# Optimization experiments

Measured on AMD Instinct MI355X. Metric: run time of the kernel, lower is better.

## Reference

```python
import jax, jax.numpy as jnp
import numpy as np

N = 200000      # nodes
E = 200000      # edges per direction
IN = 256        # in_dim
HID = 256       # hidden_dim
HEADS = 4
C = HID // HEADS  # 64 per-head channels
OUT = 128
EPS = 1e-5      # LayerNorm eps (torch default)


def _ln(x, g, b):
    m = jnp.mean(x, axis=-1, keepdims=True)
    v = jnp.mean(jnp.square(x - m), axis=-1, keepdims=True)
    return (x - m) / jnp.sqrt(v + EPS) * g + b


def _gat(x, W, att_src, att_dst, bias, edge_index):
    """PyG GATConv (default args: add_self_loops=True, negative_slope=0.2, concat heads)."""
    n = x.shape[0]
    loops = jnp.arange(n, dtype=edge_index.dtype)
    ei = jnp.concatenate([edge_index, jnp.stack([loops, loops])], axis=1)
    src, dst = ei[0], ei[1]
    h = (x @ W).reshape(n, HEADS, C)                      # [N,H,C]
    a_src = jnp.sum(h * att_src, axis=-1)                 # [N,H]
    a_dst = jnp.sum(h * att_dst, axis=-1)                 # [N,H]
    e = jax.nn.leaky_relu(a_src[src] + a_dst[dst], 0.2)   # [E+N,H]
    m = jax.ops.segment_max(e, dst, num_segments=n)       # per-dst softmax max
    ex = jnp.exp(e - m[dst])
    denom = jax.ops.segment_sum(ex, dst, num_segments=n)
    alpha = ex / denom[dst]                               # [E+N,H]
    out = jax.ops.segment_sum(h[src] * alpha[..., None], dst, num_segments=n)
    return out.reshape(n, HEADS * C) + bias


def setup_inputs() -> dict:
    key = jax.random.key(0)
    ks = jax.random.split(key, 20)
    w = lambda k, s, sc=0.05: jax.random.normal(k, s, jnp.float32) * sc
    return {
        "x": jax.random.normal(ks[0], (N, IN), jnp.float32),
        "edge_index_bu": jax.random.randint(ks[1], (2, E), 0, N, jnp.int32),
        "edge_index_td": jax.random.randint(ks[2], (2, E), 0, N, jnp.int32),
        "Wp": w(ks[3], (IN, HID)), "bp": jnp.zeros((HID,), jnp.float32),
        "W_bu": w(ks[4], (HID, HID)), "asrc_bu": w(ks[5], (HEADS, C)),
        "adst_bu": w(ks[6], (HEADS, C)), "bias_bu": jnp.zeros((HID,), jnp.float32),
        "W_td": w(ks[7], (HID, HID)), "asrc_td": w(ks[8], (HEADS, C)),
        "adst_td": w(ks[9], (HEADS, C)), "bias_td": jnp.zeros((HID,), jnp.float32),
        "Wf": w(ks[10], (2 * HID, OUT)), "bf": jnp.zeros((OUT,), jnp.float32),
        "g_bu": jnp.ones((HID,), jnp.float32), "b_bu": jnp.zeros((HID,), jnp.float32),
        "g_td": jnp.ones((HID,), jnp.float32), "b_td": jnp.zeros((HID,), jnp.float32),
        "g_out": jnp.ones((OUT,), jnp.float32), "b_out": jnp.zeros((OUT,), jnp.float32),
    }


def reference(x, edge_index_bu, edge_index_td, Wp, bp,
              W_bu, asrc_bu, adst_bu, bias_bu,
              W_td, asrc_td, adst_td, bias_td,
              Wf, bf, g_bu, b_bu, g_td, b_td, g_out, b_out):
    h = jax.nn.relu(x @ Wp + bp)  # dropout is identity in eval
    x_bu = jax.nn.relu(_ln(_gat(h, W_bu, asrc_bu, adst_bu, bias_bu, edge_index_bu), g_bu, b_bu))
    x_td = jax.nn.relu(_ln(_gat(h, W_td, asrc_td, adst_td, bias_td, edge_index_td), g_td, b_td))
    out = jnp.concatenate([x_bu, x_td], axis=-1) @ Wf + bf
    out = _ln(out, g_out, b_out)
    nrm = jnp.sqrt(jnp.sum(jnp.square(out), axis=-1, keepdims=True))
    return out / jnp.maximum(nrm, 1e-12)
```

## Files before the change

### kernel.cpp

```cpp
#include <hip/hip_runtime.h>
#include <hip/hip_bf16.h>
#include <stdint.h>


typedef __attribute__((ext_vector_type(8))) short bf16x8;
typedef __attribute__((ext_vector_type(4))) short bf16x4;
typedef __attribute__((ext_vector_type(4))) float f32x4;

#define HID 256

__device__ __forceinline__ float red16(float v) {
    #pragma unroll
    for (int o = 1; o < 16; o <<= 1) v += __shfl_xor(v, o, 64);
    return v;
}
__device__ __forceinline__ float bf2f(short s) {
    return __uint_as_float(((unsigned)(unsigned short)s) << 16);
}

__device__ __forceinline__ void gload_lds16(const void* g, void* l) {
    __builtin_amdgcn_global_load_lds(
        reinterpret_cast<const __attribute__((address_space(1))) uint32_t*>(
            reinterpret_cast<uintptr_t>(g)),
        reinterpret_cast<__attribute__((address_space(3))) uint32_t*>(
            reinterpret_cast<uintptr_t>(l)),
        16, 0, 0);
}

__global__ void transpose_w(const float* __restrict__ W,
                            __hip_bfloat16* __restrict__ Wt, int KI, int KO) {
    int idx = blockIdx.x * 256 + threadIdx.x;
    if (idx >= KI * KO) return;
    int k = idx / KO, j = idx % KO;
    Wt[(long)j * KI + k] = __float2bfloat16(W[idx]);
}

template<int BN, int MODE, int CVT>
__global__ __launch_bounds__(512) void gemm_tiled(
    const float* __restrict__ Af, const __hip_bfloat16* __restrict__ Ab, int lda,
    const __hip_bfloat16* __restrict__ Bt, int KI,
    const float* __restrict__ bias, int doRelu,
    __hip_bfloat16* __restrict__ outB, int ldcB, int colOff,
    float* __restrict__ outF,
    const float* __restrict__ gw, const float* __restrict__ bw, int N) {

    constexpr int WN = BN / 64;
    constexpr int WM = 8 / WN;
    constexpr int MR = (128 / WM) / 16;

    __shared__ __align__(16) __hip_bfloat16 sA[2][128 * 32];
    __shared__ __align__(16) __hip_bfloat16 sB[2][BN * 32];
    __shared__ float sRed[MODE == 2 ? 128 * 4 : 4];
    __shared__ float sN2[MODE == 2 ? 128 * 2 : 2];

    int tid = threadIdx.x;
    int wv = tid >> 6, ln = tid & 63;
    int m = ln & 15, q = ln >> 4;
    long row0 = (long)blockIdx.x * 128;
    int wr = (wv / WN) * (128 / WM);
    int wc = (wv % WN) * 64;

    f32x4 acc[MR][4];
    #pragma unroll
    for (int mi = 0; mi < MR; ++mi)
        #pragma unroll
        for (int t = 0; t < 4; ++t) acc[mi][t] = (f32x4){0.f, 0.f, 0.f, 0.f};

    int oA = tid * 16;
    long rowA = row0 + (oA >> 6);
    if (rowA >= N) rowA = N - 1;
    int kel = (oA & 63) >> 1;
    long aBase = rowA * (long)lda + kel;

    auto stage = [&](int buf, int k0) {
        if constexpr (CVT) {
            const float* src = Af + aBase + k0;
            f32x4 fa0 = *(const f32x4*)src;
            f32x4 fa1 = *(const f32x4*)(src + 4);
            __hip_bfloat16 t8[8];
            t8[0] = __float2bfloat16(fa0[0]); t8[1] = __float2bfloat16(fa0[1]);
            t8[2] = __float2bfloat16(fa0[2]); t8[3] = __float2bfloat16(fa0[3]);
            t8[4] = __float2bfloat16(fa1[0]); t8[5] = __float2bfloat16(fa1[1]);
            t8[6] = __float2bfloat16(fa1[2]); t8[7] = __float2bfloat16(fa1[3]);
            *(bf16x8*)((char*)sA[buf] + oA) = *(const bf16x8*)t8;
        } else {
            gload_lds16(Ab + aBase + k0, (char*)sA[buf] + oA);
        }
        #pragma unroll
        for (int j = 0; j < BN / 128; ++j) {
            int o = j * 8192 + tid * 16;
            const __hip_bfloat16* src = Bt + (long)(o >> 6) * KI + k0 + ((o & 63) >> 1);
            gload_lds16(src, (char*)sB[buf] + o);
        }
    };

    auto compute = [&](int buf) {
        bf16x8 af[MR], bfr[4];
        #pragma unroll
        for (int mi = 0; mi < MR; ++mi)
            af[mi] = *(const bf16x8*)((const char*)sA[buf] + ((wr + mi * 16 + m) << 6) + q * 16);
        #pragma unroll
        for (int t = 0; t < 4; ++t)
            bfr[t] = *(const bf16x8*)((const char*)sB[buf] + ((wc + t * 16 + m) << 6) + q * 16);
        #pragma unroll
        for (int mi = 0; mi < MR; ++mi)
            #pragma unroll
            for (int t = 0; t < 4; ++t)
                acc[mi][t] = __builtin_amdgcn_mfma_f32_16x16x32_bf16(af[mi], bfr[t],
                                                                     acc[mi][t], 0, 0, 0);
    };

    stage(0, 0);
    __syncthreads();
    int cur = 0;
    for (int k0 = 0; k0 < KI; k0 += 32) {
        if (k0 + 32 < KI) stage(cur ^ 1, k0 + 32);
        compute(cur);
        __syncthreads();
        cur ^= 1;
    }

    if constexpr (MODE != 2) {
        #pragma unroll
        for (int mi = 0; mi < MR; ++mi) {
            #pragma unroll
            for (int t = 0; t < 4; ++t) {
                int col = wc + t * 16 + m;
                float bv = bias ? bias[col] : 0.f;
                #pragma unroll
                for (int r = 0; r < 4; ++r) {
                    long row = row0 + wr + mi * 16 + q * 4 + r;
                    if (row < N) {
                        float v = acc[mi][t][r] + bv;
                        if (doRelu) v = fmaxf(v, 0.f);
                        outB[row * ldcB + colOff + col] = __float2bfloat16(v);
                    }
                }
            }
        }
    }

    if constexpr (MODE == 2) {
        float vv[MR][4][4];
        float gcol[4], bcol[4];
        #pragma unroll
        for (int t = 0; t < 4; ++t) {
            int col = wc + t * 16 + m;
            float bb = bias[col];
            gcol[t] = gw[col]; bcol[t] = bw[col];
            #pragma unroll
            for (int mi = 0; mi < MR; ++mi)
                #pragma unroll
                for (int r = 0; r < 4; ++r) vv[mi][t][r] = acc[mi][t][r] + bb;
        }
        int wcid = wc >> 6;
        __syncthreads();
        #pragma unroll
        for (int mi = 0; mi < MR; ++mi) {
            #pragma unroll
            for (int r = 0; r < 4; ++r) {
                float s1 = vv[mi][0][r] + vv[mi][1][r] + vv[mi][2][r] + vv[mi][3][r];
                float s2 = vv[mi][0][r] * vv[mi][0][r] + vv[mi][1][r] * vv[mi][1][r]
                         + vv[mi][2][r] * vv[mi][2][r] + vv[mi][3][r] * vv[mi][3][r];
                s1 = red16(s1); s2 = red16(s2);
                if (m == 0) {
                    int lrow = wr + mi * 16 + q * 4 + r;
                    sRed[lrow * 4 + wcid * 2 + 0] = s1;
                    sRed[lrow * 4 + wcid * 2 + 1] = s2;
                }
            }
        }
        __syncthreads();
        #pragma unroll
        for (int mi = 0; mi < MR; ++mi) {
            #pragma unroll
            for (int r = 0; r < 4; ++r) {
                int lrow = wr + mi * 16 + q * 4 + r;
                float S1 = sRed[lrow * 4 + 0] + sRed[lrow * 4 + 2];
                float S2 = sRed[lrow * 4 + 1] + sRed[lrow * 4 + 3];
                float mean = S1 * (1.f / 128.f);
                float var = S2 * (1.f / 128.f) - mean * mean;
                float inv = rsqrtf(fmaxf(var, 0.f) + 1e-5f);
                float n2 = 0.f;
                #pragma unroll
                for (int t = 0; t < 4; ++t) {
                    float y = (vv[mi][t][r] - mean) * inv * gcol[t] + bcol[t];
                    vv[mi][t][r] = y;
                    n2 += y * y;
                }
                n2 = red16(n2);
                if (m == 0) sN2[lrow * 2 + wcid] = n2;
            }
        }
        __syncthreads();
        #pragma unroll
        for (int mi = 0; mi < MR; ++mi) {
            #pragma unroll
            for (int r = 0; r < 4; ++r) {
                int lrow = wr + mi * 16 + q * 4 + r;
                long row = row0 + lrow;
                float nrm = sqrtf(sN2[lrow * 2] + sN2[lrow * 2 + 1]);
                float sc = 1.f / fmaxf(nrm, 1e-12f);
                if (row < N) {
                    #pragma unroll
                    for (int t = 0; t < 4; ++t)
                        outF[row * 128 + wc + t * 16 + m] = vv[mi][t][r] * sc;
                }
            }
        }
    }
}

__global__ __launch_bounds__(1024) void gemm_dir2(
    const __hip_bfloat16* __restrict__ Ab,
    const __hip_bfloat16* __restrict__ Bt,
    const float* __restrict__ asrc0, const float* __restrict__ adst0,
    const float* __restrict__ asrc1, const float* __restrict__ adst1,
    float* __restrict__ aS0, float* __restrict__ aD0,
    float* __restrict__ aS1, float* __restrict__ aD1,
    __hip_bfloat16* __restrict__ outB, int N) {
    constexpr int KI = 256;
    __shared__ __align__(16) __hip_bfloat16 sA[128 * 32];
    __shared__ __align__(16) __hip_bfloat16 sB[512 * 32];

    int tid = threadIdx.x;
    int wv = tid >> 6, ln = tid & 63;
    int m = ln & 15, q = ln >> 4;
    long row0 = (long)blockIdx.x * 128;
    int wr = (wv >> 3) * 64;
    int wc = (wv & 7) * 64;

    f32x4 acc[4][4];
    #pragma unroll
    for (int mi = 0; mi < 4; ++mi)
        #pragma unroll
        for (int t = 0; t < 4; ++t) acc[mi][t] = (f32x4){0.f, 0.f, 0.f, 0.f};

    int oA = (tid & 511) * 16;
    long rowA = row0 + (oA >> 6);
    if (rowA >= N) rowA = N - 1;
    int kel = (oA & 63) >> 1;
    long aBase = rowA * (long)KI + kel;
    int oB0 = tid * 16;
    int kelB = (oB0 & 63) >> 1;

    for (int k0 = 0; k0 < KI; k0 += 32) {
        __syncthreads();
        if (tid < 512) gload_lds16(Ab + aBase + k0, (char*)sA + oA);
        #pragma unroll
        for (int j = 0; j < 2; ++j) {
            int o = j * 16384 + oB0;
            const __hip_bfloat16* src = Bt + (long)(o >> 6) * KI + k0 + ((o & 63) >> 1);
            gload_lds16(src, (char*)sB + o);
        }
        __syncthreads();

        bf16x8 af[4], bfr[4];
        #pragma unroll
        for (int mi = 0; mi < 4; ++mi)
            af[mi] = *(const bf16x8*)((const char*)sA + ((wr + mi * 16 + m) << 6) + q * 16);
        #pragma unroll
        for (int t = 0; t < 4; ++t)
            bfr[t] = *(const bf16x8*)((const char*)sB + ((wc + t * 16 + m) << 6) + q * 16);
        #pragma unroll
        for (int mi = 0; mi < 4; ++mi)
            #pragma unroll
            for (int t = 0; t < 4; ++t)
                acc[mi][t] = __builtin_amdgcn_mfma_f32_16x16x32_bf16(af[mi], bfr[t],
                                                                     acc[mi][t], 0, 0, 0);
    }

    #pragma unroll
    for (int mi = 0; mi < 4; ++mi) {
        #pragma unroll
        for (int t = 0; t < 4; ++t) {
            int col = wc + t * 16 + m;
            #pragma unroll
            for (int r = 0; r < 4; ++r) {
                long row = row0 + wr + mi * 16 + q * 4 + r;
                if (row < N) outB[row * 512 + col] = __float2bfloat16(acc[mi][t][r]);
            }
        }
    }

    int dir = wc >> 8;
    int cc = wc & 255;
    int h = cc >> 6;
    const float* as_ = dir ? asrc1 : asrc0;
    const float* ad_ = dir ? adst1 : adst0;
    float* aS = dir ? aS1 : aS0;
    float* aD = dir ? aD1 : aD0;
    f32x4 sw, dw;
    #pragma unroll
    for (int t = 0; t < 4; ++t) {
        sw[t] = as_[cc + t * 16 + m];
        dw[t] = ad_[cc + t * 16 + m];
    }
    #pragma unroll
    for (int mi = 0; mi < 4; ++mi) {
        #pragma unroll
        for (int r = 0; r < 4; ++r) {
            float ps = acc[mi][0][r] * sw[0] + acc[mi][1][r] * sw[1]
                     + acc[mi][2][r] * sw[2] + acc[mi][3][r] * sw[3];
            float pd = acc[mi][0][r] * dw[0] + acc[mi][1][r] * dw[1]
                     + acc[mi][2][r] * dw[2] + acc[mi][3][r] * dw[3];
            ps = red16(ps); pd = red16(pd);
            long row = row0 + wr + mi * 16 + q * 4 + r;
            if (m == 0 && row < N) {
                aS[row * 4 + h] = ps;
                aD[row * 4 + h] = pd;
            }
        }
    }
}

__global__ __launch_bounds__(256) void hist_dst(const int* __restrict__ ei, int E,
                                                int* __restrict__ cnt) {
    int e = blockIdx.x * 256 + threadIdx.x;
    if (e < E) atomicAdd(&cnt[ei[E + e]], 1);
}

__global__ __launch_bounds__(256) void scan1(const int* __restrict__ cnt,
                                             int* __restrict__ offpart,
                                             int* __restrict__ bsum, int n) {
    int t = threadIdx.x, i = blockIdx.x * 256 + t;
    int lane = t & 63, w = t >> 6;
    int v = (i < n) ? cnt[i] : 0;
    int inc = v;
    #pragma unroll
    for (int o = 1; o < 64; o <<= 1) {
        int u = __shfl_up(inc, o, 64);
        if (lane >= o) inc += u;
    }
    __shared__ int wsum[4];
    if (lane == 63) wsum[w] = inc;
    __syncthreads();
    int wadd = 0;
    #pragma unroll
    for (int k = 0; k < 4; ++k) if (k < w) wadd += wsum[k];
    if (i < n) offpart[i] = inc - v + wadd;
    if (t == 255) bsum[blockIdx.x] = inc + wadd;
}

__global__ __launch_bounds__(256) void scan2(const int* __restrict__ bsum,
                                             int* __restrict__ btot, int nb) {
    int t = threadIdx.x, lane = t & 63, w = t >> 6;
    int loc[4]; int s = 0;
    #pragma unroll
    for (int k = 0; k < 4; ++k) {
        int idx = t * 4 + k;
        int v = (idx < nb) ? bsum[idx] : 0;
        loc[k] = s; s += v;
    }
    int inc = s;
    #pragma unroll
    for (int o = 1; o < 64; o <<= 1) {
        int u = __shfl_up(inc, o, 64);
        if (lane >= o) inc += u;
    }
    __shared__ int wsum[4];
    if (lane == 63) wsum[w] = inc;
    __syncthreads();
    int wadd = 0;
    #pragma unroll
    for (int k = 0; k < 4; ++k) if (k < w) wadd += wsum[k];
    int excl = inc - s + wadd;
    #pragma unroll
    for (int k = 0; k < 4; ++k) {
        int idx = t * 4 + k;
        if (idx < nb) btot[idx] = excl + loc[k];
    }
}

__global__ __launch_bounds__(256) void finalize_off(const int* __restrict__ offpart,
                                                    const int* __restrict__ btot,
                                                    int* __restrict__ off, int n, int E) {
    int i = blockIdx.x * 256 + threadIdx.x;
    if (i < n) off[i] = offpart[i] + btot[i >> 8];
    if (i == 0) off[n] = E;
}

__global__ __launch_bounds__(256) void scatter_src(const int* __restrict__ ei, int E,
                                                   const int* __restrict__ off,
                                                   int* __restrict__ cur,
                                                   int* __restrict__ esrc) {
    int e = blockIdx.x * 256 + threadIdx.x;
    if (e >= E) return;
    int d = ei[E + e];
    int pos = off[d] + atomicAdd(&cur[d], 1);
    esrc[pos] = ei[e];
}

__global__ __launch_bounds__(256) void att_alpha(
    const int* __restrict__ off, const int* __restrict__ esrc,
    const float* __restrict__ a_s, const float* __restrict__ a_d,
    float* __restrict__ alpha_self, float* __restrict__ alpha_e, int N) {
    int d = blockIdx.x * 256 + threadIdx.x;
    if (d >= N) return;
    int beg = off[d], end = off[d + 1];
    f32x4 adv = *(const f32x4*)(a_d + 4 * (long)d);
    f32x4 asd = *(const f32x4*)(a_s + 4 * (long)d);
    float es[4], m[4];
    #pragma unroll
    for (int h = 0; h < 4; ++h) {
        float e = asd[h] + adv[h]; e = e > 0.f ? e : 0.2f * e;
        es[h] = e; m[h] = e;
    }
    for (int j = beg; j < end; ++j) {
        int s = esrc[j];
        f32x4 asv = *(const f32x4*)(a_s + 4 * (long)s);
        #pragma unroll
        for (int h = 0; h < 4; ++h) {
            float e = asv[h] + adv[h]; e = e > 0.f ? e : 0.2f * e;
            m[h] = fmaxf(m[h], e);
        }
    }
    float sum[4];
    #pragma unroll
    for (int h = 0; h < 4; ++h) sum[h] = __expf(es[h] - m[h]);
    for (int j = beg; j < end; ++j) {
        int s = esrc[j];
        f32x4 asv = *(const f32x4*)(a_s + 4 * (long)s);
        #pragma unroll
        for (int h = 0; h < 4; ++h) {
            float e = asv[h] + adv[h]; e = e > 0.f ? e : 0.2f * e;
            sum[h] += __expf(e - m[h]);
        }
    }
    float rs[4];
    #pragma unroll
    for (int h = 0; h < 4; ++h) rs[h] = 1.f / sum[h];
    f32x4 sa;
    #pragma unroll
    for (int h = 0; h < 4; ++h) sa[h] = __expf(es[h] - m[h]) * rs[h];
    *(f32x4*)(alpha_self + 4 * (long)d) = sa;
    for (int j = beg; j < end; ++j) {
        int s = esrc[j];
        f32x4 asv = *(const f32x4*)(a_s + 4 * (long)s);
        f32x4 av;
        #pragma unroll
        for (int h = 0; h < 4; ++h) {
            float e = asv[h] + adv[h]; e = e > 0.f ? e : 0.2f * e;
            av[h] = __expf(e - m[h]) * rs[h];
        }
        *(f32x4*)(alpha_e + 4 * (long)j) = av;
    }
}

__global__ __launch_bounds__(256) void gat_gather(
    const int* __restrict__ off, const int* __restrict__ esrc,
    const float* __restrict__ alpha_self, const float* __restrict__ alpha_e,
    const __hip_bfloat16* __restrict__ hw, int dirOff,
    const float* __restrict__ bias, const float* __restrict__ g,
    const float* __restrict__ b,
    __hip_bfloat16* __restrict__ out, int N) {
    int tid = threadIdx.x;
    int lane = tid & 63;
    int grp = lane >> 4, li = lane & 15;
    long d = (long)blockIdx.x * 16 + (tid >> 6) * 4 + grp;
    if (d >= N) return;
    int beg = off[d], end = off[d + 1];
    int head = li >> 2;
    int c0 = li * 16;
    float acc[16];
    {
        float a = alpha_self[4 * d + head];
        const __hip_bfloat16* r = hw + d * 512 + dirOff + c0;
        bf16x8 h0 = *(const bf16x8*)r;
        bf16x8 h1 = *(const bf16x8*)(r + 8);
        #pragma unroll
        for (int k = 0; k < 8; ++k) {
            acc[k] = a * bf2f(h0[k]);
            acc[8 + k] = a * bf2f(h1[k]);
        }
    }
    for (int j = beg; j < end; ++j) {
        int s = esrc[j];
        float a = alpha_e[4 * (long)j + head];
        const __hip_bfloat16* r = hw + (long)s * 512 + dirOff + c0;
        bf16x8 h0 = *(const bf16x8*)r;
        bf16x8 h1 = *(const bf16x8*)(r + 8);
        #pragma unroll
        for (int k = 0; k < 8; ++k) {
            acc[k] += a * bf2f(h0[k]);
            acc[8 + k] += a * bf2f(h1[k]);
        }
    }
    float s1 = 0.f, s2 = 0.f;
    #pragma unroll
    for (int k = 0; k < 16; k += 4) {
        f32x4 bi = *(const f32x4*)(bias + c0 + k);
        #pragma unroll
        for (int u = 0; u < 4; ++u) {
            float v = acc[k + u] + bi[u];
            acc[k + u] = v;
            s1 += v; s2 += v * v;
        }
    }
    #pragma unroll
    for (int o = 1; o < 16; o <<= 1) {
        s1 += __shfl_xor(s1, o, 64);
        s2 += __shfl_xor(s2, o, 64);
    }
    float mean = s1 * (1.f / 256.f);
    float var = s2 * (1.f / 256.f) - mean * mean;
    float inv = rsqrtf(fmaxf(var, 0.f) + 1e-5f);
    __hip_bfloat16 o16[16];
    #pragma unroll
    for (int k = 0; k < 16; k += 4) {
        f32x4 gv = *(const f32x4*)(g + c0 + k);
        f32x4 bv = *(const f32x4*)(b + c0 + k);
        #pragma unroll
        for (int u = 0; u < 4; ++u) {
            float y = (acc[k + u] - mean) * inv * gv[u] + bv[u];
            o16[k + u] = __float2bfloat16(fmaxf(y, 0.f));
        }
    }
    __hip_bfloat16* orow = out + d * 512 + dirOff + c0;
    *(bf16x8*)orow = *(const bf16x8*)o16;
    *(bf16x8*)(orow + 8) = *(const bf16x8*)(o16 + 8);
}

extern "C" void kernel_launch(void* const* d_in, const int* in_sizes, int n_in,
                              void* d_out, int out_size, void* d_ws, size_t ws_size,
                              hipStream_t stream) {
    const float* x      = (const float*)d_in[0];
    const int*   ei_bu  = (const int*)d_in[1];
    const int*   ei_td  = (const int*)d_in[2];
    const float* Wp     = (const float*)d_in[3];
    const float* bp     = (const float*)d_in[4];
    const float* W_bu   = (const float*)d_in[5];
    const float* asrc_bu= (const float*)d_in[6];
    const float* adst_bu= (const float*)d_in[7];
    const float* bias_bu= (const float*)d_in[8];
    const float* W_td   = (const float*)d_in[9];
    const float* asrc_td= (const float*)d_in[10];
    const float* adst_td= (const float*)d_in[11];
    const float* bias_td= (const float*)d_in[12];
    const float* Wf     = (const float*)d_in[13];
    const float* bfv    = (const float*)d_in[14];
    const float* g_bu   = (const float*)d_in[15];
    const float* b_bu   = (const float*)d_in[16];
    const float* g_td   = (const float*)d_in[17];
    const float* b_td   = (const float*)d_in[18];
    const float* g_out  = (const float*)d_in[19];
    const float* b_out  = (const float*)d_in[20];

    const int N = in_sizes[0] / HID;
    const int E = in_sizes[1] / 2;

    char* ws = (char*)d_ws;
    size_t off0 = 0;
    auto take = [&](size_t bytes) -> char* {
        char* p = ws + off0;
        off0 += (bytes + 255) & ~(size_t)255;
        return p;
    };
    __hip_bfloat16* h_buf = (__hip_bfloat16*)take((size_t)N * 256 * 2);
    __hip_bfloat16* hwcat = (__hip_bfloat16*)take((size_t)N * 512 * 2);
    __hip_bfloat16* xcat  = (__hip_bfloat16*)take((size_t)N * 512 * 2);
    float* aS0   = (float*)take((size_t)N * 16);
    float* aD0   = (float*)take((size_t)N * 16);
    float* aS1   = (float*)take((size_t)N * 16);
    float* aD1   = (float*)take((size_t)N * 16);
    float* alsf  = (float*)take((size_t)N * 16);
    float* ale   = (float*)take((size_t)E * 16);
    int* cnt     = (int*)take((size_t)N * 4);
    int* cur     = (int*)take((size_t)N * 4);
    int* offpart = (int*)take((size_t)N * 4);
    int* offarr  = (int*)take((size_t)(N + 1) * 4);
    int* esrc    = (int*)take((size_t)E * 4);
    int* bsum    = (int*)take(1024 * 4);
    int* btot    = (int*)take(1024 * 4);
    __hip_bfloat16* Wpt  = (__hip_bfloat16*)take(256 * 256 * 2);
    __hip_bfloat16* Wcat = (__hip_bfloat16*)take(512 * 256 * 2);
    __hip_bfloat16* Wft  = (__hip_bfloat16*)take(128 * 512 * 2);

    transpose_w<<<(256 * 256 + 255) / 256, 256, 0, stream>>>(Wp, Wpt, 256, 256);
    transpose_w<<<(256 * 256 + 255) / 256, 256, 0, stream>>>(W_bu, Wcat, 256, 256);
    transpose_w<<<(256 * 256 + 255) / 256, 256, 0, stream>>>(W_td, Wcat + 256 * 256, 256, 256);
    transpose_w<<<(512 * 128 + 255) / 256, 256, 0, stream>>>(Wf, Wft, 512, 128);

    int gm = (N + 127) / 128;

    gemm_tiled<256, 0, 1><<<gm, 512, 0, stream>>>(
        x, nullptr, 256, Wpt, 256, bp, 1, h_buf, 256, 0, nullptr,
        nullptr, nullptr, N);

    gemm_dir2<<<gm, 1024, 0, stream>>>(
        h_buf, Wcat, asrc_bu, adst_bu, asrc_td, adst_td,
        aS0, aD0, aS1, aD1, hwcat, N);

    const int* eis[2] = {ei_bu, ei_td};
    const float* aSs[2] = {aS0, aS1};
    const float* aDs[2] = {aD0, aD1};
    const float* biases[2]= {bias_bu, bias_td};
    const float* gs[2]    = {g_bu, g_td};
    const float* bs[2]    = {b_bu, b_td};

    int egrid = (E + 255) / 256;
    int ngrid = (N + 255) / 256;
    int nb = (N + 255) / 256;
    for (int dir = 0; dir < 2; ++dir) {
        hipMemsetAsync(cnt, 0, (size_t)N * 8, stream);
        hist_dst<<<egrid, 256, 0, stream>>>(eis[dir], E, cnt);
        scan1<<<nb, 256, 0, stream>>>(cnt, offpart, bsum, N);
        scan2<<<1, 256, 0, stream>>>(bsum, btot, nb);
        finalize_off<<<ngrid, 256, 0, stream>>>(offpart, btot, offarr, N, E);
        scatter_src<<<egrid, 256, 0, stream>>>(eis[dir], E, offarr, cur, esrc);
        att_alpha<<<ngrid, 256, 0, stream>>>(offarr, esrc, aSs[dir], aDs[dir],
                                             alsf, ale, N);
        gat_gather<<<(N + 15) / 16, 256, 0, stream>>>(offarr, esrc, alsf, ale,
                                                      hwcat, dir * 256,
                                                      biases[dir], gs[dir], bs[dir],
                                                      xcat, N);
    }

    gemm_tiled<128, 2, 0><<<gm, 512, 0, stream>>>(
        nullptr, xcat, 512, Wft, 512, bfv, 0, nullptr, 128, 0, (float*)d_out,
        g_out, b_out, N);
}
```

Baseline: 871.0 us.

## Batch both GAT directions into single CSR build and gather launches

Merges the bottom-up and top-down graph pipelines into one combined graph of 2N nodes and 2E edges, with the top-down node ids offset by N. Histogram, scan, scatter, attention softmax and gather then each run once over both directions instead of twice. The intent is to halve the number of launches and memsets and to give each kernel a larger grid to fill the GPU. The cost is extra index arithmetic and per-thread direction selection inside the gather, plus a wider scan2 that handles up to 2048 block sums.

Result: faster. 841.7 us (-3.4%).

```diff
diff --git a/kernel.cpp b/kernel.cpp
--- a/kernel.cpp
+++ b/kernel.cpp
@@ -242,7 +242,6 @@
     int kel = (oA & 63) >> 1;
     long aBase = rowA * (long)KI + kel;
     int oB0 = tid * 16;
-    int kelB = (oB0 & 63) >> 1;
 
     for (int k0 = 0; k0 < KI; k0 += 32) {
         __syncthreads();
@@ -314,10 +313,12 @@
     }
 }
 
-__global__ __launch_bounds__(256) void hist_dst(const int* __restrict__ ei, int E,
-                                                int* __restrict__ cnt) {
+__global__ __launch_bounds__(256) void hist_dst2(const int* __restrict__ ei0,
+                                                 const int* __restrict__ ei1,
+                                                 int E, int N, int* __restrict__ cnt) {
     int e = blockIdx.x * 256 + threadIdx.x;
-    if (e < E) atomicAdd(&cnt[ei[E + e]], 1);
+    if (e < E) atomicAdd(&cnt[ei0[E + e]], 1);
+    else if (e < 2 * E) atomicAdd(&cnt[ei1[e] + N], 1);
 }
 
 __global__ __launch_bounds__(256) void scan1(const int* __restrict__ cnt,
@@ -345,10 +346,10 @@
 __global__ __launch_bounds__(256) void scan2(const int* __restrict__ bsum,
                                              int* __restrict__ btot, int nb) {
     int t = threadIdx.x, lane = t & 63, w = t >> 6;
-    int loc[4]; int s = 0;
-    #pragma unroll
-    for (int k = 0; k < 4; ++k) {
-        int idx = t * 4 + k;
+    int loc[8]; int s = 0;
+    #pragma unroll
+    for (int k = 0; k < 8; ++k) {
+        int idx = t * 8 + k;
         int v = (idx < nb) ? bsum[idx] : 0;
         loc[k] = s; s += v;
     }
@@ -366,37 +367,41 @@
     for (int k = 0; k < 4; ++k) if (k < w) wadd += wsum[k];
     int excl = inc - s + wadd;
     #pragma unroll
-    for (int k = 0; k < 4; ++k) {
-        int idx = t * 4 + k;
+    for (int k = 0; k < 8; ++k) {
+        int idx = t * 8 + k;
         if (idx < nb) btot[idx] = excl + loc[k];
     }
 }
 
 __global__ __launch_bounds__(256) void finalize_off(const int* __restrict__ offpart,
                                                     const int* __restrict__ btot,
-                                                    int* __restrict__ off, int n, int E) {
+                                                    int* __restrict__ off, int n, int Etot) {
     int i = blockIdx.x * 256 + threadIdx.x;
     if (i < n) off[i] = offpart[i] + btot[i >> 8];
-    if (i == 0) off[n] = E;
-}
-
-__global__ __launch_bounds__(256) void scatter_src(const int* __restrict__ ei, int E,
-                                                   const int* __restrict__ off,
-                                                   int* __restrict__ cur,
-                                                   int* __restrict__ esrc) {
+    if (i == 0) off[n] = Etot;
+}
+
+__global__ __launch_bounds__(256) void scatter_src2(const int* __restrict__ ei0,
+                                                    const int* __restrict__ ei1,
+                                                    int E, int N,
+                                                    const int* __restrict__ off,
+                                                    int* __restrict__ cur,
+                                                    int* __restrict__ esrc) {
     int e = blockIdx.x * 256 + threadIdx.x;
-    if (e >= E) return;
-    int d = ei[E + e];
+    if (e >= 2 * E) return;
+    int d, s;
+    if (e < E) { d = ei0[E + e]; s = ei0[e]; }
+    else       { d = ei1[e] + N; s = ei1[e - E] + N; }
     int pos = off[d] + atomicAdd(&cur[d], 1);
-    esrc[pos] = ei[e];
+    esrc[pos] = s;
 }
 
 __global__ __launch_bounds__(256) void att_alpha(
     const int* __restrict__ off, const int* __restrict__ esrc,
     const float* __restrict__ a_s, const float* __restrict__ a_d,
-    float* __restrict__ alpha_self, float* __restrict__ alpha_e, int N) {
+    float* __restrict__ alpha_self, float* __restrict__ alpha_e, int N2) {
     int d = blockIdx.x * 256 + threadIdx.x;
-    if (d >= N) return;
+    if (d >= N2) return;
     int beg = off[d], end = off[d + 1];
     f32x4 adv = *(const f32x4*)(a_d + 4 * (long)d);
     f32x4 asd = *(const f32x4*)(a_s + 4 * (long)d);
@@ -450,22 +455,31 @@
 __global__ __launch_bounds__(256) void gat_gather(
     const int* __restrict__ off, const int* __restrict__ esrc,
     const float* __restrict__ alpha_self, const float* __restrict__ alpha_e,
-    const __hip_bfloat16* __restrict__ hw, int dirOff,
-    const float* __restrict__ bias, const float* __restrict__ g,
-    const float* __restrict__ b,
+    const __hip_bfloat16* __restrict__ hw,
+    const float* __restrict__ bias0, const float* __restrict__ g0,
+    const float* __restrict__ b0,
+    const float* __restrict__ bias1, const float* __restrict__ g1,
+    const float* __restrict__ b1,
     __hip_bfloat16* __restrict__ out, int N) {
     int tid = threadIdx.x;
     int lane = tid & 63;
     int grp = lane >> 4, li = lane & 15;
     long d = (long)blockIdx.x * 16 + (tid >> 6) * 4 + grp;
-    if (d >= N) return;
+    if (d >= 2 * (long)N) return;
+    int dir = d >= N;
+    long dirN = (long)dir * N;
+    long pd = d - dirN;
+    int dirOff = dir << 8;
+    const float* bias = dir ? bias1 : bias0;
+    const float* g = dir ? g1 : g0;
+    const float* b = dir ? b1 : b0;
     int beg = off[d], end = off[d + 1];
     int head = li >> 2;
     int c0 = li * 16;
     float acc[16];
     {
         float a = alpha_self[4 * d + head];
-        const __hip_bfloat16* r = hw + d * 512 + dirOff + c0;
+        const __hip_bfloat16* r = hw + pd * 512 + dirOff + c0;
         bf16x8 h0 = *(const bf16x8*)r;
         bf16x8 h1 = *(const bf16x8*)(r + 8);
         #pragma unroll
@@ -475,9 +489,9 @@
         }
     }
     for (int j = beg; j < end; ++j) {
-        int s = esrc[j];
+        long s = esrc[j] - dirN;
         float a = alpha_e[4 * (long)j + head];
-        const __hip_bfloat16* r = hw + (long)s * 512 + dirOff + c0;
+        const __hip_bfloat16* r = hw + s * 512 + dirOff + c0;
         bf16x8 h0 = *(const bf16x8*)r;
         bf16x8 h1 = *(const bf16x8*)(r + 8);
         #pragma unroll
@@ -516,7 +530,7 @@
             o16[k + u] = __float2bfloat16(fmaxf(y, 0.f));
         }
     }
-    __hip_bfloat16* orow = out + d * 512 + dirOff + c0;
+    __hip_bfloat16* orow = out + pd * 512 + dirOff + c0;
     *(bf16x8*)orow = *(const bf16x8*)o16;
     *(bf16x8*)(orow + 8) = *(const bf16x8*)(o16 + 8);
 }
@@ -548,6 +562,7 @@
 
     const int N = in_sizes[0] / HID;
     const int E = in_sizes[1] / 2;
+    const int N2 = 2 * N, E2 = 2 * E;
 
     char* ws = (char*)d_ws;
     size_t off0 = 0;
@@ -559,19 +574,17 @@
     __hip_bfloat16* h_buf = (__hip_bfloat16*)take((size_t)N * 256 * 2);
     __hip_bfloat16* hwcat = (__hip_bfloat16*)take((size_t)N * 512 * 2);
     __hip_bfloat16* xcat  = (__hip_bfloat16*)take((size_t)N * 512 * 2);
-    float* aS0   = (float*)take((size_t)N * 16);
-    float* aD0   = (float*)take((size_t)N * 16);
-    float* aS1   = (float*)take((size_t)N * 16);
-    float* aD1   = (float*)take((size_t)N * 16);
-    float* alsf  = (float*)take((size_t)N * 16);
-    float* ale   = (float*)take((size_t)E * 16);
-    int* cnt     = (int*)take((size_t)N * 4);
-    int* cur     = (int*)take((size_t)N * 4);
-    int* offpart = (int*)take((size_t)N * 4);
-    int* offarr  = (int*)take((size_t)(N + 1) * 4);
-    int* esrc    = (int*)take((size_t)E * 4);
-    int* bsum    = (int*)take(1024 * 4);
-    int* btot    = (int*)take(1024 * 4);
+    float* aS    = (float*)take((size_t)N2 * 16);
+    float* aD    = (float*)take((size_t)N2 * 16);
+    float* alsf  = (float*)take((size_t)N2 * 16);
+    float* ale   = (float*)take((size_t)E2 * 16);
+    int* cnt     = (int*)take((size_t)N2 * 4);
+    int* cur     = (int*)take((size_t)N2 * 4);
+    int* offpart = (int*)take((size_t)N2 * 4);
+    int* offarr  = (int*)take((size_t)(N2 + 1) * 4);
+    int* esrc    = (int*)take((size_t)E2 * 4);
+    int* bsum    = (int*)take(2048 * 4);
+    int* btot    = (int*)take(2048 * 4);
     __hip_bfloat16* Wpt  = (__hip_bfloat16*)take(256 * 256 * 2);
     __hip_bfloat16* Wcat = (__hip_bfloat16*)take(512 * 256 * 2);
     __hip_bfloat16* Wft  = (__hip_bfloat16*)take(128 * 512 * 2);
@@ -589,32 +602,21 @@
 
     gemm_dir2<<<gm, 1024, 0, stream>>>(
         h_buf, Wcat, asrc_bu, adst_bu, asrc_td, adst_td,
-        aS0, aD0, aS1, aD1, hwcat, N);
-
-    const int* eis[2] = {ei_bu, ei_td};
-    const float* aSs[2] = {aS0, aS1};
-    const float* aDs[2] = {aD0, aD1};
-    const float* biases[2]= {bias_bu, bias_td};
-    const float* gs[2]    = {g_bu, g_td};
-    const float* bs[2]    = {b_bu, b_td};
-
-    int egrid = (E + 255) / 256;
-    int ngrid = (N + 255) / 256;
-    int nb = (N + 255) / 256;
-    for (int dir = 0; dir < 2; ++dir) {
-        hipMemsetAsync(cnt, 0, (size_t)N * 8, stream);
-        hist_dst<<<egrid, 256, 0, stream>>>(eis[dir], E, cnt);
-        scan1<<<nb, 256, 0, stream>>>(cnt, offpart, bsum, N);
-        scan2<<<1, 256, 0, stream>>>(bsum, btot, nb);
-        finalize_off<<<ngrid, 256, 0, stream>>>(offpart, btot, offarr, N, E);
-        scatter_src<<<egrid, 256, 0, stream>>>(eis[dir], E, offarr, cur, esrc);
-        att_alpha<<<ngrid, 256, 0, stream>>>(offarr, esrc, aSs[dir], aDs[dir],
-                                             alsf, ale, N);
-        gat_gather<<<(N + 15) / 16, 256, 0, stream>>>(offarr, esrc, alsf, ale,
-                                                      hwcat, dir * 256,
-                                                      biases[dir], gs[dir], bs[dir],
-                                                      xcat, N);
-    }
+        aS, aD, aS + (size_t)N * 4, aD + (size_t)N * 4, hwcat, N);
+
+    int egrid2 = (E2 + 255) / 256;
+    int ngrid2 = (N2 + 255) / 256;
+    hipMemsetAsync(cnt, 0, (size_t)N2 * 8, stream);
+    hist_dst2<<<egrid2, 256, 0, stream>>>(ei_bu, ei_td, E, N, cnt);
+    scan1<<<ngrid2, 256, 0, stream>>>(cnt, offpart, bsum, N2);
+    scan2<<<1, 256, 0, stream>>>(bsum, btot, ngrid2);
+    finalize_off<<<ngrid2, 256, 0, stream>>>(offpart, btot, offarr, N2, E2);
+    scatter_src2<<<egrid2, 256, 0, stream>>>(ei_bu, ei_td, E, N, offarr, cur, esrc);
+    att_alpha<<<ngrid2, 256, 0, stream>>>(offarr, esrc, aS, aD, alsf, ale, N2);
+    gat_gather<<<(N2 + 15) / 16, 256, 0, stream>>>(offarr, esrc, alsf, ale, hwcat,
+                                                   bias_bu, g_bu, b_bu,
+                                                   bias_td, g_td, b_td,
+                                                   xcat, N);
 
     gemm_tiled<128, 2, 0><<<gm, 512, 0, stream>>>(
         nullptr, xcat, 512, Wft, 512, bfv, 0, nullptr, 128, 0, (float*)d_out,
```
